# Performance work log

Measured on AMD Instinct MI355X. Metric: run time of the kernel, lower is better.

Reference implementation:

```python
import jax, jax.numpy as jnp
import numpy as np

N = 500_000
B = 10_000
D = 256
H = 256
NODES_PER_GRAPH = N // B
BN_EPS = 1e-5


def setup_inputs() -> dict:
    key = jax.random.key(0)
    ks = jax.random.split(key, 8)
    s = 1.0 / np.sqrt(D)
    feat = jax.random.normal(ks[0], (N, D), dtype=jnp.float32)
    intend = jax.random.normal(ks[1], (B, D), dtype=jnp.float32)
    # B graphs of equal size; sorted segment ids, last node of each graph
    segment_ids = jnp.repeat(jnp.arange(B, dtype=jnp.int32), NODES_PER_GRAPH)
    last_nodes = (jnp.arange(B, dtype=jnp.int32) + 1) * NODES_PER_GRAPH - 1
    return {
        "feat": feat,
        "intend": intend,
        "last_nodes": last_nodes,
        "segment_ids": segment_ids,
        "W_u": jax.random.uniform(ks[2], (D, H), jnp.float32, -s, s),
        "W_v": jax.random.uniform(ks[3], (D, H), jnp.float32, -s, s),
        "b_v": jnp.zeros((H,), jnp.float32),
        "W_i": jax.random.uniform(ks[4], (D, H), jnp.float32, -s, s),
        "b_i": jnp.zeros((H,), jnp.float32),
        "W_e": jax.random.uniform(ks[5], (H, 1), jnp.float32, -1.0 / np.sqrt(H), 1.0 / np.sqrt(H)),
        "bn_gamma": jnp.ones((D,), jnp.float32),
        "bn_beta": jnp.zeros((D,), jnp.float32),
        "bn_mean": jnp.zeros((D,), jnp.float32),
        "bn_var": jnp.ones((D,), jnp.float32),
    }


def reference(feat, intend, last_nodes, segment_ids, W_u, W_v, b_v, W_i, b_i, W_e,
              bn_gamma, bn_beta, bn_mean, bn_var):
    num_graphs = intend.shape[0]
    # BatchNorm1d in eval mode (running stats)
    feat = (feat - bn_mean) * (bn_gamma / jnp.sqrt(bn_var + BN_EPS)) + bn_beta
    # dropout p=0.0 -> identity
    feat_u = feat @ W_u                                   # [N, H]
    last_emb = feat[last_nodes] @ W_i + b_i               # [B, H]
    feat_v = intend @ W_v + b_v                           # [B, H]
    per_graph = last_emb + feat_v                         # [B, H]
    # broadcast_nodes: gather per-graph vectors to nodes
    gate = jax.nn.sigmoid(feat_u + per_graph[segment_ids])  # [N, H]
    e = (gate @ W_e)[:, 0]                                # [N]
    # ragged segment softmax
    m = jax.ops.segment_max(e, segment_ids, num_segments=num_graphs)
    ex = jnp.exp(e - m[segment_ids])
    denom = jax.ops.segment_sum(ex, segment_ids, num_segments=num_graphs)
    alpha = ex / denom[segment_ids]                       # [N]
    # weighted segment-sum readout
    rst = jax.ops.segment_sum(feat * alpha[:, None], segment_ids, num_segments=num_graphs)
    # output_dim == input_dim -> fc_out is None; activation is None
    return rst
```

## Files before the change

kernel.cpp:

```cpp
#include <hip/hip_runtime.h>
#include <stdint.h>

typedef short short8 __attribute__((ext_vector_type(8)));
typedef float f32x4 __attribute__((ext_vector_type(4)));

#define NPG   50
#define GPB   2
#define ROWS  100
#define MP    112
#define MT    7
#define LDA   264
#define BN_EPS 1e-5f

__device__ __forceinline__ float bf2f(unsigned short u) {
    union { unsigned int i; float f; } v; v.i = ((unsigned int)u) << 16; return v.f;
}
__device__ __forceinline__ unsigned short f2bf(float f) {
    union { float f; unsigned int i; } v; v.f = f;
    unsigned int i = v.i;
    return (unsigned short)((i + 0x7FFFu + ((i >> 16) & 1u)) >> 16);
}

__global__ void prep_kernel(const float* __restrict__ Wu,
                            const float* __restrict__ Wv,
                            const float* __restrict__ Wi,
                            const float* __restrict__ bv,
                            const float* __restrict__ bi,
                            const float* __restrict__ gamma,
                            const float* __restrict__ beta,
                            const float* __restrict__ mean,
                            const float* __restrict__ var,
                            float* __restrict__ sc, float* __restrict__ sh,
                            float* __restrict__ bias_iv,
                            unsigned short* __restrict__ Wt,
                            unsigned short* __restrict__ Wt2) {
    int gid = blockIdx.x * 256 + threadIdx.x;
    int k = gid >> 8, n = gid & 255;
    Wt [n * 256 + k]       = f2bf(Wu[k * 256 + n]);
    Wt2[n * 512 + k]       = f2bf(Wi[k * 256 + n]);
    Wt2[n * 512 + 256 + k] = f2bf(Wv[k * 256 + n]);
    if (gid < 256) {
        float s = gamma[gid] * rsqrtf(var[gid] + BN_EPS);
        sc[gid] = s;
        sh[gid] = beta[gid] - mean[gid] * s;
        bias_iv[gid] = bi[gid] + bv[gid];
    }
}

__global__ __launch_bounds__(256) void pgraph_kernel(
    const float* __restrict__ feat,
    const float* __restrict__ intend,
    const int* __restrict__ last_nodes,
    const unsigned short* __restrict__ Wt2,
    const float* __restrict__ sc, const float* __restrict__ sh,
    const float* __restrict__ bias_iv,
    unsigned short* __restrict__ Pb, int Bnum) {
    __shared__ unsigned short A2[64 * 520];

    int tid = threadIdx.x;
    int g0 = blockIdx.x * 64;
    int cg = tid & 31, k0 = cg * 8;
    float scv[8], shv[8];
#pragma unroll
    for (int j = 0; j < 8; ++j) { scv[j] = sc[k0 + j]; shv[j] = sh[k0 + j]; }

    for (int t = tid; t < 64 * 32; t += 256) {
        int row = t >> 5;
        int g = g0 + row; if (g > Bnum - 1) g = Bnum - 1;
        int ln = last_nodes[g];
        const float* src = feat + (size_t)ln * 256 + k0;
        float4 u0 = *(const float4*)(src);
        float4 u1 = *(const float4*)(src + 4);
        float f[8] = {u0.x, u0.y, u0.z, u0.w, u1.x, u1.y, u1.z, u1.w};
        unsigned int o[4];
#pragma unroll
        for (int m = 0; m < 4; ++m) {
            unsigned short lo = f2bf(f[2*m]   * scv[2*m]   + shv[2*m]);
            unsigned short hi = f2bf(f[2*m+1] * scv[2*m+1] + shv[2*m+1]);
            o[m] = (unsigned int)lo | ((unsigned int)hi << 16);
        }
        *(uint4*)(&A2[row * 520 + k0]) = make_uint4(o[0], o[1], o[2], o[3]);
    }
    for (int t = tid; t < 64 * 32; t += 256) {
        int row = t >> 5;
        int g = g0 + row; if (g > Bnum - 1) g = Bnum - 1;
        const float* src = intend + (size_t)g * 256 + k0;
        float4 u0 = *(const float4*)(src);
        float4 u1 = *(const float4*)(src + 4);
        float f[8] = {u0.x, u0.y, u0.z, u0.w, u1.x, u1.y, u1.z, u1.w};
        unsigned int o[4];
#pragma unroll
        for (int m = 0; m < 4; ++m)
            o[m] = (unsigned int)f2bf(f[2*m]) | ((unsigned int)f2bf(f[2*m+1]) << 16);
        *(uint4*)(&A2[row * 520 + 256 + k0]) = make_uint4(o[0], o[1], o[2], o[3]);
    }
    __syncthreads();

    int w = tid >> 6, l = tid & 63, lm = l & 15, lq = l >> 4;
    int nbase = w * 64;
    float bias4[4];
#pragma unroll
    for (int nt = 0; nt < 4; ++nt) bias4[nt] = bias_iv[nbase + nt*16 + lm];

    for (int mt = 0; mt < 4; ++mt) {
        f32x4 acc[4];
#pragma unroll
        for (int nt = 0; nt < 4; ++nt) acc[nt] = (f32x4){0.f, 0.f, 0.f, 0.f};
#pragma unroll
        for (int ks = 0; ks < 16; ++ks) {
            short8 a = *(const short8*)(&A2[(mt*16 + lm) * 520 + ks*32 + lq*8]);
#pragma unroll
            for (int nt = 0; nt < 4; ++nt) {
                short8 b = *(const short8*)(Wt2 + (size_t)(nbase + nt*16 + lm) * 512 + ks*32 + lq*8);
                acc[nt] = __builtin_amdgcn_mfma_f32_16x16x32_bf16(a, b, acc[nt], 0, 0, 0);
            }
        }
#pragma unroll
        for (int nt = 0; nt < 4; ++nt) {
            int col = nbase + nt*16 + lm;
#pragma unroll
            for (int r = 0; r < 4; ++r) {
                int row = mt*16 + lq*4 + r;
                int g = g0 + row;
                if (g < Bnum) Pb[(size_t)g * 256 + col] = f2bf(acc[nt][r] + bias4[nt]);
            }
        }
    }
}

__global__ __launch_bounds__(256, 2) void main_kernel(
    const float* __restrict__ feat,
    const unsigned short* __restrict__ Wt,
    const float* __restrict__ We,
    const float* __restrict__ sc, const float* __restrict__ sh,
    const unsigned short* __restrict__ Pb,
    float* __restrict__ out) {
    __shared__ unsigned short featA[MP * LDA];
    __shared__ float P_lds[GPB][256];
    __shared__ float e_parts[4][MP];
    __shared__ float e_lds[MP];
    __shared__ float alpha_lds[MP];
    __shared__ float red[8][GPB][256];

    int tid = threadIdx.x;
    int w = tid >> 6, l = tid & 63, lm = l & 15, lq = l >> 4;
    int nbase = w * 64;
    size_t row0 = (size_t)blockIdx.x * ROWS;

    short8 bfr[4][8];
#pragma unroll
    for (int nt = 0; nt < 4; ++nt)
#pragma unroll
        for (int ks = 0; ks < 8; ++ks)
            bfr[nt][ks] = *(const short8*)(Wt + (size_t)(nbase + nt*16 + lm) * 256 + ks*32 + lq*8);
    float we4[4];
#pragma unroll
    for (int nt = 0; nt < 4; ++nt) we4[nt] = We[nbase + nt*16 + lm];

    int cg = tid & 31, k0 = cg * 8;
    float scv[8], shv[8];
#pragma unroll
    for (int j = 0; j < 8; ++j) { scv[j] = sc[k0 + j]; shv[j] = sh[k0 + j]; }
    for (int t = tid; t < ROWS * 32; t += 256) {
        int row = t >> 5;
        const float* src = feat + (row0 + row) * 256 + k0;
        float4 u0 = *(const float4*)(src);
        float4 u1 = *(const float4*)(src + 4);
        float f[8] = {u0.x, u0.y, u0.z, u0.w, u1.x, u1.y, u1.z, u1.w};
        unsigned int o[4];
#pragma unroll
        for (int m = 0; m < 4; ++m) {
            unsigned short lo = f2bf(f[2*m]   * scv[2*m]   + shv[2*m]);
            unsigned short hi = f2bf(f[2*m+1] * scv[2*m+1] + shv[2*m+1]);
            o[m] = (unsigned int)lo | ((unsigned int)hi << 16);
        }
        *(uint4*)(&featA[row * LDA + k0]) = make_uint4(o[0], o[1], o[2], o[3]);
    }
    for (int t = tid; t < (MP - ROWS) * 32; t += 256) {
        int row = ROWS + (t >> 5);
        int c0 = (t & 31) * 8;
        *(uint4*)(&featA[row * LDA + c0]) = make_uint4(0u, 0u, 0u, 0u);
    }
    for (int t = tid; t < GPB * 256; t += 256)
        ((float*)P_lds)[t] = bf2f(Pb[(size_t)blockIdx.x * GPB * 256 + t]);
    __syncthreads();

    for (int mt = 0; mt < MT; ++mt) {
        f32x4 acc[4];
#pragma unroll
        for (int nt = 0; nt < 4; ++nt) acc[nt] = (f32x4){0.f, 0.f, 0.f, 0.f};
#pragma unroll
        for (int ks = 0; ks < 8; ++ks) {
            short8 a = *(const short8*)(&featA[(mt*16 + lm) * LDA + ks*32 + lq*8]);
#pragma unroll
            for (int nt = 0; nt < 4; ++nt)
                acc[nt] = __builtin_amdgcn_mfma_f32_16x16x32_bf16(a, bfr[nt][ks], acc[nt], 0, 0, 0);
        }
        float er[4] = {0.f, 0.f, 0.f, 0.f};
#pragma unroll
        for (int nt = 0; nt < 4; ++nt) {
            int col = nbase + nt*16 + lm;
            float pw = we4[nt];
#pragma unroll
            for (int r = 0; r < 4; ++r) {
                int row = mt*16 + lq*4 + r;
                int lg = (row >= NPG) ? 1 : 0;
                float g = acc[nt][r] + P_lds[lg][col];
                float s = __builtin_amdgcn_rcpf(1.0f + __expf(-g));
                er[r] += s * pw;
            }
        }
#pragma unroll
        for (int r = 0; r < 4; ++r)
#pragma unroll
            for (int mask = 1; mask < 16; mask <<= 1)
                er[r] += __shfl_xor(er[r], mask, 64);
        if (lm == 0) {
#pragma unroll
            for (int r = 0; r < 4; ++r)
                e_parts[w][mt*16 + lq*4 + r] = er[r];
        }
    }
    __syncthreads();
    if (tid < MP)
        e_lds[tid] = e_parts[0][tid] + e_parts[1][tid] + e_parts[2][tid] + e_parts[3][tid];
    __syncthreads();

    if (w < GPB) {
        float ev = (l < NPG) ? e_lds[w * NPG + l] : -3.0e38f;
        float m = ev;
#pragma unroll
        for (int mask = 1; mask < 64; mask <<= 1) m = fmaxf(m, __shfl_xor(m, mask, 64));
        float p = (l < NPG) ? __expf(ev - m) : 0.f;
        float s = p;
#pragma unroll
        for (int mask = 1; mask < 64; mask <<= 1) s += __shfl_xor(s, mask, 64);
        if (l < NPG) alpha_lds[w * NPG + l] = p * __builtin_amdgcn_rcpf(s);
    }
    __syncthreads();

    int rl = tid >> 5;
    float a0[8], a1[8];
#pragma unroll
    for (int j = 0; j < 8; ++j) { a0[j] = 0.f; a1[j] = 0.f; }
    for (int i = rl; i < ROWS; i += 8) {
        float al = alpha_lds[i];
        uint4 u = *(const uint4*)(&featA[i * LDA + k0]);
        unsigned int uu[4] = {u.x, u.y, u.z, u.w};
        float f[8];
#pragma unroll
        for (int m = 0; m < 4; ++m) {
            f[2*m]   = bf2f((unsigned short)(uu[m] & 0xFFFFu));
            f[2*m+1] = bf2f((unsigned short)(uu[m] >> 16));
        }
        if (i < NPG) {
#pragma unroll
            for (int j = 0; j < 8; ++j) a0[j] += al * f[j];
        } else {
#pragma unroll
            for (int j = 0; j < 8; ++j) a1[j] += al * f[j];
        }
    }
#pragma unroll
    for (int j = 0; j < 8; ++j) { red[rl][0][k0 + j] = a0[j]; red[rl][1][k0 + j] = a1[j]; }
    __syncthreads();
    {
        int col = tid;
#pragma unroll
        for (int lg = 0; lg < GPB; ++lg) {
            float s = 0.f;
#pragma unroll
            for (int r = 0; r < 8; ++r) s += red[r][lg][col];
            out[(size_t)(blockIdx.x * GPB + lg) * 256 + col] = s;
        }
    }
}

extern "C" void kernel_launch(void* const* d_in, const int* in_sizes, int n_in,
                              void* d_out, int out_size, void* d_ws, size_t ws_size,
                              hipStream_t stream) {
    const float* feat      = (const float*)d_in[0];
    const float* intend    = (const float*)d_in[1];
    const int* last_nodes  = (const int*)d_in[2];
    const float* Wu    = (const float*)d_in[4];
    const float* Wv    = (const float*)d_in[5];
    const float* bv    = (const float*)d_in[6];
    const float* Wi    = (const float*)d_in[7];
    const float* bi    = (const float*)d_in[8];
    const float* We    = (const float*)d_in[9];
    const float* gamma = (const float*)d_in[10];
    const float* beta  = (const float*)d_in[11];
    const float* mean  = (const float*)d_in[12];
    const float* var   = (const float*)d_in[13];

    int Bnum = in_sizes[2];

    char* ws = (char*)d_ws;
    float* sc       = (float*)ws;
    float* sh       = (float*)(ws + 1024);
    float* bias_iv  = (float*)(ws + 2048);
    unsigned short* Wt  = (unsigned short*)(ws + 4096);
    unsigned short* Wt2 = (unsigned short*)(ws + 4096 + 131072);
    unsigned short* Pb  = (unsigned short*)(ws + 4096 + 131072 + 262144);

    prep_kernel<<<256, 256, 0, stream>>>(Wu, Wv, Wi, bv, bi, gamma, beta, mean, var,
                                         sc, sh, bias_iv, Wt, Wt2);
    pgraph_kernel<<<(Bnum + 63) / 64, 256, 0, stream>>>(feat, intend, last_nodes, Wt2,
                                                        sc, sh, bias_iv, Pb, Bnum);
    main_kernel<<<Bnum / GPB, 256, 0, stream>>>(feat, Wt, We, sc, sh, Pb,
                                                (float*)d_out);
}
```

Baseline: 855.6 us.

## Fold BatchNorm into weights and make main kernel persistent over graph tiles

The BatchNorm scale is folded into the bf16 W_u and W_i weights, and the shift becomes a precomputed per-column gate constant. The readout then applies scale and shift once per output instead of once per element, since the softmax weights sum to one. This removes the per-element normalize in the feature load. The main kernel becomes persistent: 500 blocks loop over the 5000 tiles and load the W_u register fragments once per block instead of once per tile, at the cost of an extra small kernel and per-tile barriers.

```diff
diff --git a/kernel.cpp b/kernel.cpp
--- a/kernel.cpp
+++ b/kernel.cpp
@@ -1,4 +1,5 @@
 #include <hip/hip_runtime.h>
+#include <hip/hip_bf16.h>
 #include <stdint.h>
 
 typedef short short8 __attribute__((ext_vector_type(8)));
@@ -10,6 +11,8 @@
 #define MP    112
 #define MT    7
 #define LDA   264
+#define NTILES 5000
+#define MAIN_GRID 500
 #define BN_EPS 1e-5f
 
 __device__ __forceinline__ float bf2f(unsigned short u) {
@@ -20,31 +23,49 @@
     unsigned int i = v.i;
     return (unsigned short)((i + 0x7FFFu + ((i >> 16) & 1u)) >> 16);
 }
+__device__ __forceinline__ unsigned int pack_bf16(float a, float b) {
+    __hip_bfloat162 h = __float22bfloat162_rn(make_float2(a, b));
+    unsigned int o; __builtin_memcpy(&o, &h, 4); return o;
+}
 
 __global__ void prep_kernel(const float* __restrict__ Wu,
                             const float* __restrict__ Wv,
                             const float* __restrict__ Wi,
-                            const float* __restrict__ bv,
-                            const float* __restrict__ bi,
                             const float* __restrict__ gamma,
                             const float* __restrict__ beta,
                             const float* __restrict__ mean,
                             const float* __restrict__ var,
                             float* __restrict__ sc, float* __restrict__ sh,
-                            float* __restrict__ bias_iv,
                             unsigned short* __restrict__ Wt,
                             unsigned short* __restrict__ Wt2) {
-    int gid = blockIdx.x * 256 + threadIdx.x;
-    int k = gid >> 8, n = gid & 255;
-    Wt [n * 256 + k]       = f2bf(Wu[k * 256 + n]);
-    Wt2[n * 512 + k]       = f2bf(Wi[k * 256 + n]);
+    int k = blockIdx.x, n = threadIdx.x;
+    float s = gamma[k] * rsqrtf(var[k] + BN_EPS);
+    Wt [n * 256 + k]       = f2bf(s * Wu[k * 256 + n]);
+    Wt2[n * 512 + k]       = f2bf(s * Wi[k * 256 + n]);
     Wt2[n * 512 + 256 + k] = f2bf(Wv[k * 256 + n]);
-    if (gid < 256) {
-        float s = gamma[gid] * rsqrtf(var[gid] + BN_EPS);
-        sc[gid] = s;
-        sh[gid] = beta[gid] - mean[gid] * s;
-        bias_iv[gid] = bi[gid] + bv[gid];
-    }
+    if (k == 0) {
+        float sn = gamma[n] * rsqrtf(var[n] + BN_EPS);
+        sc[n] = sn;
+        sh[n] = beta[n] - mean[n] * sn;
+    }
+}
+
+__global__ __launch_bounds__(256) void gconst_kernel(
+    const float* __restrict__ Wu, const float* __restrict__ Wi,
+    const float* __restrict__ bi, const float* __restrict__ bv,
+    const float* __restrict__ gamma, const float* __restrict__ beta,
+    const float* __restrict__ mean, const float* __restrict__ var,
+    float* __restrict__ gt) {
+    __shared__ float r4[4];
+    int n = blockIdx.x, k = threadIdx.x;
+    float s = gamma[k] * rsqrtf(var[k] + BN_EPS);
+    float shk = beta[k] - mean[k] * s;
+    float p = shk * (Wu[k * 256 + n] + Wi[k * 256 + n]);
+#pragma unroll
+    for (int mask = 1; mask < 64; mask <<= 1) p += __shfl_xor(p, mask, 64);
+    if ((k & 63) == 0) r4[k >> 6] = p;
+    __syncthreads();
+    if (k == 0) gt[n] = r4[0] + r4[1] + r4[2] + r4[3] + bi[n] + bv[n];
 }
 
 __global__ __launch_bounds__(256) void pgraph_kernel(
@@ -52,17 +73,13 @@
     const float* __restrict__ intend,
     const int* __restrict__ last_nodes,
     const unsigned short* __restrict__ Wt2,
-    const float* __restrict__ sc, const float* __restrict__ sh,
-    const float* __restrict__ bias_iv,
+    const float* __restrict__ gt,
     unsigned short* __restrict__ Pb, int Bnum) {
     __shared__ unsigned short A2[64 * 520];
 
     int tid = threadIdx.x;
     int g0 = blockIdx.x * 64;
-    int cg = tid & 31, k0 = cg * 8;
-    float scv[8], shv[8];
-#pragma unroll
-    for (int j = 0; j < 8; ++j) { scv[j] = sc[k0 + j]; shv[j] = sh[k0 + j]; }
+    int k0 = (tid & 31) * 8;
 
     for (int t = tid; t < 64 * 32; t += 256) {
         int row = t >> 5;
@@ -71,15 +88,9 @@
         const float* src = feat + (size_t)ln * 256 + k0;
         float4 u0 = *(const float4*)(src);
         float4 u1 = *(const float4*)(src + 4);
-        float f[8] = {u0.x, u0.y, u0.z, u0.w, u1.x, u1.y, u1.z, u1.w};
-        unsigned int o[4];
-#pragma unroll
-        for (int m = 0; m < 4; ++m) {
-            unsigned short lo = f2bf(f[2*m]   * scv[2*m]   + shv[2*m]);
-            unsigned short hi = f2bf(f[2*m+1] * scv[2*m+1] + shv[2*m+1]);
-            o[m] = (unsigned int)lo | ((unsigned int)hi << 16);
-        }
-        *(uint4*)(&A2[row * 520 + k0]) = make_uint4(o[0], o[1], o[2], o[3]);
+        *(uint4*)(&A2[row * 520 + k0]) = make_uint4(
+            pack_bf16(u0.x, u0.y), pack_bf16(u0.z, u0.w),
+            pack_bf16(u1.x, u1.y), pack_bf16(u1.z, u1.w));
     }
     for (int t = tid; t < 64 * 32; t += 256) {
         int row = t >> 5;
@@ -87,12 +98,9 @@
         const float* src = intend + (size_t)g * 256 + k0;
         float4 u0 = *(const float4*)(src);
         float4 u1 = *(const float4*)(src + 4);
-        float f[8] = {u0.x, u0.y, u0.z, u0.w, u1.x, u1.y, u1.z, u1.w};
-        unsigned int o[4];
-#pragma unroll
-        for (int m = 0; m < 4; ++m)
-            o[m] = (unsigned int)f2bf(f[2*m]) | ((unsigned int)f2bf(f[2*m+1]) << 16);
-        *(uint4*)(&A2[row * 520 + 256 + k0]) = make_uint4(o[0], o[1], o[2], o[3]);
+        *(uint4*)(&A2[row * 520 + 256 + k0]) = make_uint4(
+            pack_bf16(u0.x, u0.y), pack_bf16(u0.z, u0.w),
+            pack_bf16(u1.x, u1.y), pack_bf16(u1.z, u1.w));
     }
     __syncthreads();
 
@@ -100,7 +108,7 @@
     int nbase = w * 64;
     float bias4[4];
 #pragma unroll
-    for (int nt = 0; nt < 4; ++nt) bias4[nt] = bias_iv[nbase + nt*16 + lm];
+    for (int nt = 0; nt < 4; ++nt) bias4[nt] = gt[nbase + nt*16 + lm];
 
     for (int mt = 0; mt < 4; ++mt) {
         f32x4 acc[4];
@@ -145,7 +153,8 @@
     int tid = threadIdx.x;
     int w = tid >> 6, l = tid & 63, lm = l & 15, lq = l >> 4;
     int nbase = w * 64;
-    size_t row0 = (size_t)blockIdx.x * ROWS;
+    int k0 = (tid & 31) * 8;
+    int rl = tid >> 5;
 
     short8 bfr[4][8];
 #pragma unroll
@@ -156,123 +165,120 @@
     float we4[4];
 #pragma unroll
     for (int nt = 0; nt < 4; ++nt) we4[nt] = We[nbase + nt*16 + lm];
-
-    int cg = tid & 31, k0 = cg * 8;
-    float scv[8], shv[8];
-#pragma unroll
-    for (int j = 0; j < 8; ++j) { scv[j] = sc[k0 + j]; shv[j] = sh[k0 + j]; }
-    for (int t = tid; t < ROWS * 32; t += 256) {
-        int row = t >> 5;
-        const float* src = feat + (row0 + row) * 256 + k0;
-        float4 u0 = *(const float4*)(src);
-        float4 u1 = *(const float4*)(src + 4);
-        float f[8] = {u0.x, u0.y, u0.z, u0.w, u1.x, u1.y, u1.z, u1.w};
-        unsigned int o[4];
-#pragma unroll
-        for (int m = 0; m < 4; ++m) {
-            unsigned short lo = f2bf(f[2*m]   * scv[2*m]   + shv[2*m]);
-            unsigned short hi = f2bf(f[2*m+1] * scv[2*m+1] + shv[2*m+1]);
-            o[m] = (unsigned int)lo | ((unsigned int)hi << 16);
-        }
-        *(uint4*)(&featA[row * LDA + k0]) = make_uint4(o[0], o[1], o[2], o[3]);
-    }
+    float sc_c = sc[tid], sh_c = sh[tid];
+
     for (int t = tid; t < (MP - ROWS) * 32; t += 256) {
         int row = ROWS + (t >> 5);
         int c0 = (t & 31) * 8;
         *(uint4*)(&featA[row * LDA + c0]) = make_uint4(0u, 0u, 0u, 0u);
     }
-    for (int t = tid; t < GPB * 256; t += 256)
-        ((float*)P_lds)[t] = bf2f(Pb[(size_t)blockIdx.x * GPB * 256 + t]);
-    __syncthreads();
-
-    for (int mt = 0; mt < MT; ++mt) {
-        f32x4 acc[4];
-#pragma unroll
-        for (int nt = 0; nt < 4; ++nt) acc[nt] = (f32x4){0.f, 0.f, 0.f, 0.f};
-#pragma unroll
-        for (int ks = 0; ks < 8; ++ks) {
-            short8 a = *(const short8*)(&featA[(mt*16 + lm) * LDA + ks*32 + lq*8]);
-#pragma unroll
-            for (int nt = 0; nt < 4; ++nt)
-                acc[nt] = __builtin_amdgcn_mfma_f32_16x16x32_bf16(a, bfr[nt][ks], acc[nt], 0, 0, 0);
-        }
-        float er[4] = {0.f, 0.f, 0.f, 0.f};
-#pragma unroll
-        for (int nt = 0; nt < 4; ++nt) {
-            int col = nbase + nt*16 + lm;
-            float pw = we4[nt];
-#pragma unroll
-            for (int r = 0; r < 4; ++r) {
-                int row = mt*16 + lq*4 + r;
-                int lg = (row >= NPG) ? 1 : 0;
-                float g = acc[nt][r] + P_lds[lg][col];
-                float s = __builtin_amdgcn_rcpf(1.0f + __expf(-g));
-                er[r] += s * pw;
-            }
-        }
-#pragma unroll
-        for (int r = 0; r < 4; ++r)
-#pragma unroll
-            for (int mask = 1; mask < 16; mask <<= 1)
-                er[r] += __shfl_xor(er[r], mask, 64);
-        if (lm == 0) {
+
+    for (int tile = blockIdx.x; tile < NTILES; tile += MAIN_GRID) {
+        size_t row0 = (size_t)tile * ROWS;
+
+        for (int t = tid; t < ROWS * 32; t += 256) {
+            int row = t >> 5;
+            int c0 = (t & 31) * 8;
+            const float* src = feat + (row0 + row) * 256 + c0;
+            float4 u0 = *(const float4*)(src);
+            float4 u1 = *(const float4*)(src + 4);
+            *(uint4*)(&featA[row * LDA + c0]) = make_uint4(
+                pack_bf16(u0.x, u0.y), pack_bf16(u0.z, u0.w),
+                pack_bf16(u1.x, u1.y), pack_bf16(u1.z, u1.w));
+        }
+        for (int t = tid; t < GPB * 256; t += 256)
+            ((float*)P_lds)[t] = bf2f(Pb[(size_t)tile * GPB * 256 + t]);
+        __syncthreads();
+
+        for (int mt = 0; mt < MT; ++mt) {
+            f32x4 acc[4];
+#pragma unroll
+            for (int nt = 0; nt < 4; ++nt) acc[nt] = (f32x4){0.f, 0.f, 0.f, 0.f};
+#pragma unroll
+            for (int ks = 0; ks < 8; ++ks) {
+                short8 a = *(const short8*)(&featA[(mt*16 + lm) * LDA + ks*32 + lq*8]);
+#pragma unroll
+                for (int nt = 0; nt < 4; ++nt)
+                    acc[nt] = __builtin_amdgcn_mfma_f32_16x16x32_bf16(a, bfr[nt][ks], acc[nt], 0, 0, 0);
+            }
+            float er[4] = {0.f, 0.f, 0.f, 0.f};
+#pragma unroll
+            for (int nt = 0; nt < 4; ++nt) {
+                int col = nbase + nt*16 + lm;
+                float pw = we4[nt];
+#pragma unroll
+                for (int r = 0; r < 4; ++r) {
+                    int row = mt*16 + lq*4 + r;
+                    int lg = (row >= NPG) ? 1 : 0;
+                    float g = acc[nt][r] + P_lds[lg][col];
+                    float s = __builtin_amdgcn_rcpf(1.0f + __expf(-g));
+                    er[r] += s * pw;
+                }
+            }
 #pragma unroll
             for (int r = 0; r < 4; ++r)
-                e_parts[w][mt*16 + lq*4 + r] = er[r];
-        }
-    }
-    __syncthreads();
-    if (tid < MP)
-        e_lds[tid] = e_parts[0][tid] + e_parts[1][tid] + e_parts[2][tid] + e_parts[3][tid];
-    __syncthreads();
-
-    if (w < GPB) {
-        float ev = (l < NPG) ? e_lds[w * NPG + l] : -3.0e38f;
-        float m = ev;
-#pragma unroll
-        for (int mask = 1; mask < 64; mask <<= 1) m = fmaxf(m, __shfl_xor(m, mask, 64));
-        float p = (l < NPG) ? __expf(ev - m) : 0.f;
-        float s = p;
-#pragma unroll
-        for (int mask = 1; mask < 64; mask <<= 1) s += __shfl_xor(s, mask, 64);
-        if (l < NPG) alpha_lds[w * NPG + l] = p * __builtin_amdgcn_rcpf(s);
-    }
-    __syncthreads();
-
-    int rl = tid >> 5;
-    float a0[8], a1[8];
-#pragma unroll
-    for (int j = 0; j < 8; ++j) { a0[j] = 0.f; a1[j] = 0.f; }
-    for (int i = rl; i < ROWS; i += 8) {
-        float al = alpha_lds[i];
-        uint4 u = *(const uint4*)(&featA[i * LDA + k0]);
-        unsigned int uu[4] = {u.x, u.y, u.z, u.w};
-        float f[8];
-#pragma unroll
-        for (int m = 0; m < 4; ++m) {
-            f[2*m]   = bf2f((unsigned short)(uu[m] & 0xFFFFu));
-            f[2*m+1] = bf2f((unsigned short)(uu[m] >> 16));
-        }
-        if (i < NPG) {
-#pragma unroll
-            for (int j = 0; j < 8; ++j) a0[j] += al * f[j];
-        } else {
-#pragma unroll
-            for (int j = 0; j < 8; ++j) a1[j] += al * f[j];
-        }
-    }
-#pragma unroll
-    for (int j = 0; j < 8; ++j) { red[rl][0][k0 + j] = a0[j]; red[rl][1][k0 + j] = a1[j]; }
-    __syncthreads();
-    {
-        int col = tid;
-#pragma unroll
-        for (int lg = 0; lg < GPB; ++lg) {
-            float s = 0.f;
-#pragma unroll
-            for (int r = 0; r < 8; ++r) s += red[r][lg][col];
-            out[(size_t)(blockIdx.x * GPB + lg) * 256 + col] = s;
-        }
+#pragma unroll
+                for (int mask = 1; mask < 16; mask <<= 1)
+                    er[r] += __shfl_xor(er[r], mask, 64);
+            if (lm == 0) {
+#pragma unroll
+                for (int r = 0; r < 4; ++r)
+                    e_parts[w][mt*16 + lq*4 + r] = er[r];
+            }
+        }
+        __syncthreads();
+        if (tid < MP)
+            e_lds[tid] = e_parts[0][tid] + e_parts[1][tid] + e_parts[2][tid] + e_parts[3][tid];
+        __syncthreads();
+
+        if (w < GPB) {
+            float ev = (l < NPG) ? e_lds[w * NPG + l] : -3.0e38f;
+            float m = ev;
+#pragma unroll
+            for (int mask = 1; mask < 64; mask <<= 1) m = fmaxf(m, __shfl_xor(m, mask, 64));
+            float p = (l < NPG) ? __expf(ev - m) : 0.f;
+            float s = p;
+#pragma unroll
+            for (int mask = 1; mask < 64; mask <<= 1) s += __shfl_xor(s, mask, 64);
+            if (l < NPG) alpha_lds[w * NPG + l] = p * __builtin_amdgcn_rcpf(s);
+        }
+        __syncthreads();
+
+        float a0[8], a1[8];
+#pragma unroll
+        for (int j = 0; j < 8; ++j) { a0[j] = 0.f; a1[j] = 0.f; }
+        for (int i = rl; i < ROWS; i += 8) {
+            float al = alpha_lds[i];
+            uint4 u = *(const uint4*)(&featA[i * LDA + k0]);
+            unsigned int uu[4] = {u.x, u.y, u.z, u.w};
+            float f[8];
+#pragma unroll
+            for (int m = 0; m < 4; ++m) {
+                f[2*m]   = bf2f((unsigned short)(uu[m] & 0xFFFFu));
+                f[2*m+1] = bf2f((unsigned short)(uu[m] >> 16));
+            }
+            if (i < NPG) {
+#pragma unroll
+                for (int j = 0; j < 8; ++j) a0[j] += al * f[j];
+            } else {
+#pragma unroll
+                for (int j = 0; j < 8; ++j) a1[j] += al * f[j];
+            }
+        }
+#pragma unroll
+        for (int j = 0; j < 8; ++j) { red[rl][0][k0 + j] = a0[j]; red[rl][1][k0 + j] = a1[j]; }
+        __syncthreads();
+        {
+            int col = tid;
+#pragma unroll
+            for (int lg = 0; lg < GPB; ++lg) {
+                float s = 0.f;
+#pragma unroll
+                for (int r = 0; r < 8; ++r) s += red[r][lg][col];
+                out[(size_t)(tile * GPB + lg) * 256 + col] = sc_c * s + sh_c;
+            }
+        }
+        __syncthreads();
     }
 }
 
@@ -296,17 +302,16 @@
     int Bnum = in_sizes[2];
 
     char* ws = (char*)d_ws;
-    float* sc       = (float*)ws;
-    float* sh       = (float*)(ws + 1024);
-    float* bias_iv  = (float*)(ws + 2048);
+    float* sc = (float*)ws;
+    float* sh = (float*)(ws + 1024);
+    float* gt = (float*)(ws + 2048);
     unsigned short* Wt  = (unsigned short*)(ws + 4096);
     unsigned short* Wt2 = (unsigned short*)(ws + 4096 + 131072);
     unsigned short* Pb  = (unsigned short*)(ws + 4096 + 131072 + 262144);
 
-    prep_kernel<<<256, 256, 0, stream>>>(Wu, Wv, Wi, bv, bi, gamma, beta, mean, var,
-                                         sc, sh, bias_iv, Wt, Wt2);
+    prep_kernel<<<256, 256, 0, stream>>>(Wu, Wv, Wi, gamma, beta, mean, var, sc, sh, Wt, Wt2);
+    gconst_kernel<<<256, 256, 0, stream>>>(Wu, Wi, bi, bv, gamma, beta, mean, var, gt);
     pgraph_kernel<<<(Bnum + 63) / 64, 256, 0, stream>>>(feat, intend, last_nodes, Wt2,
-                                                        sc, sh, bias_iv, Pb, Bnum);
-    main_kernel<<<Bnum / GPB, 256, 0, stream>>>(feat, Wt, We, sc, sh, Pb,
-                                                (float*)d_out);
-}
+                                                        gt, Pb, Bnum);
+    main_kernel<<<MAIN_GRID, 256, 0, stream>>>(feat, Wt, We, sc, sh, Pb, (float*)d_out);
+}
```

New measurement: 814.5 us. 4.8% less time.
